# Kernel optimization log

Measured on AMD Instinct MI355X. Metric: run time of the kernel, lower is better.

## Reference

```python
import jax, jax.numpy as jnp
import numpy as np

N_PRIORS = 262144
N_CLASSES = 81  # includes background at index 0


def _decode(loc, priors, variance):
    # Standard SSD decode: priors are [N,4] (cx, cy, w, h) in relative coords.
    centers = priors[:, :2] + loc[:, :2] * variance[0] * priors[:, 2:]
    sizes = priors[:, 2:] * jnp.exp(loc[:, 2:] * variance[1])
    mins = centers - sizes * 0.5          # (xmin, ymin)
    maxs = mins + sizes                   # (xmax, ymax)
    return jnp.concatenate([mins, maxs], axis=-1)  # [N,4]


def setup_inputs() -> dict:
    key = jax.random.key(0)
    k1, k2, k3 = jax.random.split(key, 3)
    inp = jax.random.normal(k1, (1, N_PRIORS, 4 + N_CLASSES), dtype=jnp.float32)
    cxy = jax.random.uniform(k2, (N_PRIORS, 2), dtype=jnp.float32)
    wh = jax.random.uniform(k3, (N_PRIORS, 2), dtype=jnp.float32) * 0.1 + 0.05
    priors = jnp.concatenate([cxy, wh], axis=-1)
    variance = jnp.array([0.1, 0.2], dtype=jnp.float32)
    score_threshold = jnp.array([0.3], dtype=jnp.float32)
    return {"input": inp, "priors": priors, "variance": variance,
            "score_threshold": score_threshold}


def reference(input, priors, variance, score_threshold):
    # input: [1, N, 4+C]
    loc = input[0, :, :4]                                   # [N,4]
    cls = jax.nn.softmax(input[0, :, 4:], axis=-1)          # [N,C]
    class_conf = jnp.max(cls, axis=1)                       # [N]
    class_pred = jnp.argmax(cls, axis=1)                    # [N] int
    boxes = _decode(loc, priors, variance)                  # [N,4]
    # torch version compacts via nonzero/index_select; jit-compatible
    # equivalent: keep fixed length N and mask out invalid rows.
    valid = (class_pred > 0) & (class_conf > score_threshold[0])  # [N] bool
    boxes = jnp.where(valid[:, None], boxes, 0.0)
    class_conf = jnp.where(valid, class_conf, 0.0)
    class_pred_out = jnp.where(valid, class_pred - 1, -1)
    detections = jnp.concatenate(
        [boxes, class_conf[:, None], class_pred_out[:, None].astype(jnp.float32)],
        axis=-1)                                            # [N,6]
    return boxes, class_conf, class_pred_out, detections[None]
```

## Files before the change

kernel.cpp:

```cpp
#include <hip/hip_runtime.h>

#define NCLS 81
#define ROW  85
#define TPB  64
#define BLK_BYTES (TPB * ROW * 4)

typedef __attribute__((address_space(3))) void*       as3_void;
typedef const __attribute__((address_space(1))) void* as1_cvoid;

__device__ __forceinline__ float exp_cr(float xf) {
    double x = (double)xf;
    x = (x < -150.0) ? -150.0 : x;
    double t = x * 1.4426950408889634074;
    double nd = rint(t);
    double r = fma(nd, -6.93147180369123816490e-01, x);
    r = fma(nd, -1.90821492927058770002e-10, r);
    double p = 1.0 / 6227020800.0;
    p = fma(p, r, 1.0 / 479001600.0);
    p = fma(p, r, 1.0 / 39916800.0);
    p = fma(p, r, 1.0 / 3628800.0);
    p = fma(p, r, 1.0 / 362880.0);
    p = fma(p, r, 1.0 / 40320.0);
    p = fma(p, r, 1.0 / 5040.0);
    p = fma(p, r, 1.0 / 720.0);
    p = fma(p, r, 1.0 / 120.0);
    p = fma(p, r, 1.0 / 24.0);
    p = fma(p, r, 1.0 / 6.0);
    p = fma(p, r, 0.5);
    p = fma(p, r, 1.0);
    p = fma(p, r, 1.0);
    long long ni = (long long)nd;
    double sc = __longlong_as_double((1023LL + ni) << 52);
    return (float)(p * sc);
}

__global__ __launch_bounds__(TPB) void ssd_decode_kernel(
    const float* __restrict__ inp,
    const float* __restrict__ priors,
    const float* __restrict__ var,
    const float* __restrict__ thr,
    float* __restrict__ out,
    int n)
{
    __shared__ __align__(16) float lds[TPB * ROW];
    const int tid = threadIdx.x;
    const long long base = (long long)blockIdx.x * TPB;
    if (base >= n) return;

    {
        const char* gsrc = (const char*)inp + (long long)blockIdx.x * BLK_BYTES;
        char* lbase = (char*)lds;
        #pragma unroll
        for (int k = 0; k < 21; ++k) {
            __builtin_amdgcn_global_load_lds(
                (as1_cvoid)(gsrc + k * 1024 + tid * 16),
                (as3_void)(lbase + k * 1024), 16, 0, 0);
        }
        __builtin_amdgcn_global_load_lds(
            (as1_cvoid)(gsrc + 21504 + tid * 4),
            (as3_void)(lbase + 21504), 4, 0, 0);
        asm volatile("s_waitcnt vmcnt(0)" ::: "memory");
        __builtin_amdgcn_sched_barrier(0);
    }
    __syncthreads();

    float* row = lds + tid * ROW;

    float mx[8];
    #pragma unroll
    for (int j = 0; j < 8; ++j) mx[j] = row[4 + j];
    #pragma unroll
    for (int k = 1; k < 10; ++k)
        #pragma unroll
        for (int j = 0; j < 8; ++j) mx[j] = fmaxf(mx[j], row[4 + k * 8 + j]);
    float m = fmaxf(fmaxf(fmaxf(mx[0], mx[1]), fmaxf(mx[2], mx[3])),
                    fmaxf(fmaxf(mx[4], mx[5]), fmaxf(mx[6], mx[7])));
    m = fmaxf(m, row[84]);

    float racc[8];
    #pragma unroll
    for (int j = 0; j < 8; ++j) racc[j] = 0.0f;
    #pragma unroll
    for (int k = 0; k < 10; ++k)
        #pragma unroll
        for (int j = 0; j < 8; ++j) {
            float e = exp_cr(row[4 + k * 8 + j] - m);
            row[4 + k * 8 + j] = e;
            racc[j] += e;
        }
    float s = ((racc[0] + racc[1]) + (racc[2] + racc[3]))
            + ((racc[4] + racc[5]) + (racc[6] + racc[7]));
    float e80 = exp_cr(row[84] - m);
    row[84] = e80;
    s += e80;

    float pmax = 1.0f / s;
    float t = 1.0f;
    #pragma unroll
    for (int k = 0; k < 8; ++k) {
        float tn = __uint_as_float(__float_as_uint(t) - 1u);
        t = ((tn / s) == pmax) ? tn : t;
    }

    int am = 81;
    #pragma unroll
    for (int c = 80; c >= 0; --c)
        am = (row[4 + c] >= t) ? c : am;

    float l0 = row[0], l1 = row[1], l2 = row[2], l3 = row[3];
    float4 pr = reinterpret_cast<const float4*>(priors)[base + tid];
    float v0 = var[0], v1 = var[1];
    float cx = pr.x + l0 * v0 * pr.z;
    float cy = pr.y + l1 * v0 * pr.w;
    float w  = pr.z * exp_cr(l2 * v1);
    float h  = pr.w * exp_cr(l3 * v1);
    float x0 = cx - w * 0.5f;
    float y0 = cy - h * 0.5f;
    float x1 = x0 + w;
    float y1 = y0 + h;

    bool valid = (am > 0) && (pmax > thr[0]);

    float4 box;
    box.x = valid ? x0 : 0.0f;
    box.y = valid ? y0 : 0.0f;
    box.z = valid ? x1 : 0.0f;
    box.w = valid ? y1 : 0.0f;
    float cz = valid ? pmax : 0.0f;
    float pz = valid ? (float)(am - 1) : -1.0f;

    const long long i = base + tid;
    reinterpret_cast<float4*>(out)[i] = box;
    out[(long long)4 * n + i] = cz;
    out[(long long)5 * n + i] = pz;
    float2* det2 = reinterpret_cast<float2*>(out + (long long)6 * n + i * 6);
    det2[0] = make_float2(box.x, box.y);
    det2[1] = make_float2(box.z, box.w);
    det2[2] = make_float2(cz, pz);
}

extern "C" void kernel_launch(void* const* d_in, const int* in_sizes, int n_in,
                              void* d_out, int out_size, void* d_ws, size_t ws_size,
                              hipStream_t stream)
{
    const float* inp    = (const float*)d_in[0];
    const float* priors = (const float*)d_in[1];
    const float* var    = (const float*)d_in[2];
    const float* thr    = (const float*)d_in[3];
    float* out = (float*)d_out;

    int n = in_sizes[1] / 4;
    int blocks = (n + TPB - 1) / TPB;
    ssd_decode_kernel<<<blocks, TPB, 0, stream>>>(inp, priors, var, thr, out, n);
}
```

Baseline: 149.9 us.

## Use fast exp with wave-uniform fallback to exact softmax path for near-ties

Computes softmax sums with fast hardware __expf and finds the argmax directly from the max logit. The slow correctly-rounded double-precision exp path runs only when some lane in the wavefront has a near-tie at the max. Box decoding also switches to __expf. This removes most of the double-precision exp cost, but the confidence and box values may differ slightly from the reference rounding.

```diff
diff --git a/kernel.cpp b/kernel.cpp
--- a/kernel.cpp
+++ b/kernel.cpp
@@ -77,6 +77,8 @@
                     fmaxf(fmaxf(mx[4], mx[5]), fmaxf(mx[6], mx[7])));
     m = fmaxf(m, row[84]);
 
+    int nc = 0;
+    int amf = 127;
     float racc[8];
     #pragma unroll
     for (int j = 0; j < 8; ++j) racc[j] = 0.0f;
@@ -84,49 +86,80 @@
     for (int k = 0; k < 10; ++k)
         #pragma unroll
         for (int j = 0; j < 8; ++j) {
-            float e = exp_cr(row[4 + k * 8 + j] - m);
-            row[4 + k * 8 + j] = e;
-            racc[j] += e;
+            int c = k * 8 + j;
+            float d = row[4 + c] - m;
+            nc  += (d >= -9.5367431640625e-07f) ? 1 : 0;
+            int cand = (d == 0.0f) ? c : 127;
+            amf = (cand < amf) ? cand : amf;
+            racc[j] += __expf(d);
         }
-    float s = ((racc[0] + racc[1]) + (racc[2] + racc[3]))
-            + ((racc[4] + racc[5]) + (racc[6] + racc[7]));
-    float e80 = exp_cr(row[84] - m);
-    row[84] = e80;
-    s += e80;
-
-    float pmax = 1.0f / s;
-    float t = 1.0f;
-    #pragma unroll
-    for (int k = 0; k < 8; ++k) {
-        float tn = __uint_as_float(__float_as_uint(t) - 1u);
-        t = ((tn / s) == pmax) ? tn : t;
+    float s1 = ((racc[0] + racc[1]) + (racc[2] + racc[3]))
+             + ((racc[4] + racc[5]) + (racc[6] + racc[7]));
+    {
+        float d80 = row[84] - m;
+        nc  += (d80 >= -9.5367431640625e-07f) ? 1 : 0;
+        int cand = (d80 == 0.0f) ? 80 : 127;
+        amf = (cand < amf) ? cand : amf;
+        s1 += __expf(d80);
     }
 
-    int am = 81;
-    #pragma unroll
-    for (int c = 80; c >= 0; --c)
-        am = (row[4 + c] >= t) ? c : am;
+    int am;
+    float conf;
+    if (__any(nc > 1)) {
+        float racx[8];
+        #pragma unroll
+        for (int j = 0; j < 8; ++j) racx[j] = 0.0f;
+        #pragma unroll
+        for (int k = 0; k < 10; ++k)
+            #pragma unroll
+            for (int j = 0; j < 8; ++j) {
+                float e = exp_cr(row[4 + k * 8 + j] - m);
+                row[4 + k * 8 + j] = e;
+                racx[j] += e;
+            }
+        float s = ((racx[0] + racx[1]) + (racx[2] + racx[3]))
+                + ((racx[4] + racx[5]) + (racx[6] + racx[7]));
+        float e80 = exp_cr(row[84] - m);
+        row[84] = e80;
+        s += e80;
+
+        float pmax = 1.0f / s;
+        float t = 1.0f;
+        #pragma unroll
+        for (int k = 0; k < 8; ++k) {
+            float tn = __uint_as_float(__float_as_uint(t) - 1u);
+            t = ((tn / s) == pmax) ? tn : t;
+        }
+        am = 81;
+        #pragma unroll
+        for (int c = 80; c >= 0; --c)
+            am = (row[4 + c] >= t) ? c : am;
+        conf = pmax;
+    } else {
+        am = amf;
+        conf = 1.0f / s1;
+    }
 
     float l0 = row[0], l1 = row[1], l2 = row[2], l3 = row[3];
     float4 pr = reinterpret_cast<const float4*>(priors)[base + tid];
     float v0 = var[0], v1 = var[1];
     float cx = pr.x + l0 * v0 * pr.z;
     float cy = pr.y + l1 * v0 * pr.w;
-    float w  = pr.z * exp_cr(l2 * v1);
-    float h  = pr.w * exp_cr(l3 * v1);
+    float w  = pr.z * __expf(l2 * v1);
+    float h  = pr.w * __expf(l3 * v1);
     float x0 = cx - w * 0.5f;
     float y0 = cy - h * 0.5f;
     float x1 = x0 + w;
     float y1 = y0 + h;
 
-    bool valid = (am > 0) && (pmax > thr[0]);
+    bool valid = (am > 0) && (conf > thr[0]);
 
     float4 box;
     box.x = valid ? x0 : 0.0f;
     box.y = valid ? y0 : 0.0f;
     box.z = valid ? x1 : 0.0f;
     box.w = valid ? y1 : 0.0f;
-    float cz = valid ? pmax : 0.0f;
+    float cz = valid ? conf : 0.0f;
     float pz = valid ? (float)(am - 1) : -1.0f;
 
     const long long i = base + tid;
```

Result: faster. 144.6 us (-3.5%).
